# Kernel tuning notes

Measured on AMD Instinct MI355X. Metric: run time of the kernel, lower is better.

Reference implementation:

```python
import jax, jax.numpy as jnp
import numpy as np


def setup_inputs() -> dict:
    key = jax.random.key(0)
    k1, k2, k3 = jax.random.split(key, 3)
    B, Cin, Cout, K, H, W = 4, 64, 64, 3, 160, 160
    inputs = jax.random.normal(k1, (B, Cin, H, W), dtype=jnp.float32)
    # fractional dilation rates in [1, 3]
    rate_map = 1.0 + 2.0 * jax.random.uniform(k2, (B, 1, H, W), dtype=jnp.float32)
    # xavier-uniform-ish init
    limit = float(np.sqrt(6.0 / (Cin * K * K + Cout * K * K)))
    weight = jax.random.uniform(k3, (Cout, Cin, K, K), dtype=jnp.float32,
                                minval=-limit, maxval=limit)
    bias = jnp.zeros((Cout,), dtype=jnp.float32)
    return {"inputs": inputs, "weight": weight, "rate_map": rate_map,
            "bias": bias, "stride_h": 1, "stride_w": 1}


def _pdconv2d(inputs, weight, rate_map, bias, stride_h, stride_w):
    """Perspective (fractional, per-pixel) dilated conv with same padding.

    For each output pixel, the KxK taps are placed at center + offset*rate,
    where rate comes from rate_map and may be fractional -> bilinear sampling
    with zeros outside the image.
    """
    B, C, H, W = inputs.shape
    O, _, K, _ = weight.shape
    HO = (H + stride_h - 1) // stride_h
    WO = (W + stride_w - 1) // stride_w

    rate = rate_map[:, 0, ::stride_h, ::stride_w]  # [B,HO,WO]
    cy = (jnp.arange(HO) * stride_h).astype(jnp.float32)
    cx = (jnp.arange(WO) * stride_w).astype(jnp.float32)
    off = jnp.arange(K, dtype=jnp.float32) - (K - 1) / 2.0  # centered taps

    # sampling coords [B,HO,WO,K,K]
    sy = cy[None, :, None, None, None] + off[None, None, None, :, None] * rate[:, :, :, None, None]
    sx = cx[None, None, :, None, None] + off[None, None, None, None, :] * rate[:, :, :, None, None]
    sy = jnp.broadcast_to(sy, (B, HO, WO, K, K))
    sx = jnpp = jnp.broadcast_to(sx, (B, HO, WO, K, K))
    sx = jnp_p = sx  # no-op alias (keeps names clear)

    y0 = jnp.floor(sy)
    x0 = jnp.floor(sx)
    wy = sy - y0  # bilinear weights
    wx = sx - x0
    y0i = y0.astype(jnp.int32)
    x0i = x0.astype(jnp.int32)

    img = inputs.reshape(B, C, H * W)

    def gather(idx):  # idx [B,HO,WO,K,K] -> [B,C,HO,WO,K,K]
        return jax.vmap(lambda im, ix: jnp.take(im, ix, axis=-1))(img, idx)

    acc = jnp.zeros((B, C, HO, WO, K, K), dtype=inputs.dtype)
    corners = [(0, 0, (1 - wy) * (1 - wx)), (0, 1, (1 - wy) * wx),
               (1, 0, wy * (1 - wx)), (1, 1, wy * wx)]
    for dy, dx, cw in corners:
        yy = y0i + dy
        xx = x0i + dx
        valid = (yy >= 0) & (yy < H) & (xx >= 0) & (xx < W)
        idx = jnp.clip(yy, 0, H - 1) * W + jnp.clip(xx, 0, W - 1)
        w = (cw * valid.astype(inputs.dtype))[:, None]  # [B,1,HO,WO,K,K]
        acc = acc + gather(idx) * w

    # [B,C,HO,WO,K,K] x [O,C,K,K] -> [B,O,HO,WO]
    out = jnp.einsum('bchwkl,ockl->bohw', acc, weight)
    return out + bias[None, :, None, None]


def reference(inputs, weight, rate_map, bias, stride_h, stride_w):
    return _pdconv2d(inputs, weight, rate_map, bias, stride_h, stride_w)
```

## Files before the change

kernel.cpp:

```cpp
#include <hip/hip_runtime.h>
#include <hip/hip_bf16.h>

#define NB   4
#define CIN  64
#define COUT 64
#define HH   160
#define WW   160
#define HW   (HH * WW)

#define RT   8
#define CT   22
#define RS   72
#define RSB  (RS * 2)
#define HIN_SHORTS (RT * CT * RS)

typedef __attribute__((ext_vector_type(8))) short bf16x8;
typedef __attribute__((ext_vector_type(4))) float f32x4;
typedef __attribute__((ext_vector_type(2))) float f32x2;
typedef __attribute__((ext_vector_type(4))) unsigned int u32x4;

static __device__ __forceinline__ short f2bf(float v) {
    return __builtin_bit_cast(short, __float2bfloat16(v));
}

__global__ void wtf_kernel(const float* __restrict__ w, short* __restrict__ wtf) {
    int i = blockIdx.x * 256 + threadIdx.x;
    if (i < 36864) {
        const int j  = i & 7;
        const int l  = (i >> 3) & 63;
        const int mt = (i >> 9) & 3;
        const int ks = (i >> 11) & 1;
        const int t  = i >> 12;
        const int o  = 16 * mt + (l & 15);
        const int c  = 32 * ks + 8 * (l >> 4) + j;
        wtf[i] = f2bf(w[(o * CIN + c) * 9 + t]);
    }
}

static __device__ __forceinline__ void consume_tap(
    const u32x4 v00, const u32x4 v01, const u32x4 v10, const u32x4 v11,
    const float c00, const float c01, const float c10, const float c11,
    const bf16x8 wf0, const bf16x8 wf1, const bf16x8 wf2, const bf16x8 wf3,
    f32x4 acc[4])
{
    union { bf16x8 v; unsigned u[4]; } pf;
#pragma unroll
    for (int wd = 0; wd < 4; ++wd) {
        f32x2 s;
        {
            const unsigned u0 = v00[wd];
            const f32x2 xv = { __builtin_bit_cast(float, u0 << 16),
                               __builtin_bit_cast(float, u0 & 0xffff0000u) };
            s = c00 * xv;
        }
        {
            const unsigned u0 = v01[wd];
            const f32x2 xv = { __builtin_bit_cast(float, u0 << 16),
                               __builtin_bit_cast(float, u0 & 0xffff0000u) };
            s += c01 * xv;
        }
        {
            const unsigned u0 = v10[wd];
            const f32x2 xv = { __builtin_bit_cast(float, u0 << 16),
                               __builtin_bit_cast(float, u0 & 0xffff0000u) };
            s += c10 * xv;
        }
        {
            const unsigned u0 = v11[wd];
            const f32x2 xv = { __builtin_bit_cast(float, u0 << 16),
                               __builtin_bit_cast(float, u0 & 0xffff0000u) };
            s += c11 * xv;
        }
        unsigned r;
        asm("v_cvt_pk_bf16_f32 %0, %1, %2" : "=v"(r) : "v"(s.x), "v"(s.y));
        pf.u[wd] = r;
    }
    acc[0] = __builtin_amdgcn_mfma_f32_16x16x32_bf16(wf0, pf.v, acc[0], 0, 0, 0);
    acc[1] = __builtin_amdgcn_mfma_f32_16x16x32_bf16(wf1, pf.v, acc[1], 0, 0, 0);
    acc[2] = __builtin_amdgcn_mfma_f32_16x16x32_bf16(wf2, pf.v, acc[2], 0, 0, 0);
    acc[3] = __builtin_amdgcn_mfma_f32_16x16x32_bf16(wf3, pf.v, acc[3], 0, 0, 0);
}

__global__ __launch_bounds__(256, 4) void pdconv_tile_kernel(
    const float* __restrict__ in,
    const short* __restrict__ wtf,
    const float* __restrict__ rate_map,
    const float* __restrict__ bias,
    float* __restrict__ out)
{
    __shared__ short hin[HIN_SHORTS];
    __shared__ float red[2][64][17];

    const int tid  = threadIdx.x;
    const int wave = tid >> 6;
    const int lane = tid & 63;
    const int px   = lane & 15;
    const int g    = lane >> 4;
    const int r    = wave >> 1;
    const int th   = wave & 1;

    const int cpx = gridDim.x >> 3;
    const int bid = (blockIdx.x & 7) * cpx + (blockIdx.x >> 3);

    const int b   = bid / 800;
    const int rem = bid - b * 800;
    const int rr  = rem / 10;
    const int cc  = rem - rr * 10;
    const int oy  = 2 * rr - 3;
    const int ox  = 16 * cc - 3;

    if (tid < RT * CT) {
        const int ty = tid / CT;
        const int tx = tid - ty * CT;
        const int gy = min(max(oy + ty, 0), HH - 1);
        const int gx = min(max(ox + tx, 0), WW - 1);
        const float* src = in + (size_t)b * CIN * HW + gy * WW + gx;
        short* dst = hin + tid * RS;
#pragma unroll 16
        for (int c = 0; c < CIN; ++c)
            dst[c] = f2bf(src[(size_t)c * HW]);
    }

    const int row = 2 * rr + r;
    const int x   = 16 * cc + px;
    const float rate = rate_map[b * HW + row * WW + x];
    const float fy = (float)row, fx = (float)x;

    float wy0v[3], wy1v[3];  int ryb[3];
#pragma unroll
    for (int ky = 0; ky < 3; ++ky) {
        const float sy  = fy + (float)(ky - 1) * rate;
        const float y0f = floorf(sy);
        const float wy  = sy - y0f;
        const int   y0  = (int)y0f;
        const float vy0 = (y0 >= 0 && y0 < HH) ? 1.0f : 0.0f;
        const float vy1 = (y0 + 1 >= 0 && y0 + 1 < HH) ? 1.0f : 0.0f;
        wy0v[ky] = (1.0f - wy) * vy0;
        wy1v[ky] = wy * vy1;
        ryb[ky]  = (y0 - oy) * (CT * RSB);
    }
    float wx0v[3], wx1v[3];  int txb[3];
#pragma unroll
    for (int kx = 0; kx < 3; ++kx) {
        const float sx  = fx + (float)(kx - 1) * rate;
        const float x0f = floorf(sx);
        const float wx  = sx - x0f;
        const int   x0  = (int)x0f;
        const float vx0 = (x0 >= 0 && x0 < WW) ? 1.0f : 0.0f;
        const float vx1 = (x0 + 1 >= 0 && x0 + 1 < WW) ? 1.0f : 0.0f;
        wx0v[kx] = (1.0f - wx) * vx0;
        wx1v[kx] = wx * vx1;
        txb[kx]  = (x0 - ox) * RSB;
    }

    const int chan_off = 32 * th + 8 * g;

    const short* wtb = wtf + lane * 8;

    f32x4 acc[4];
#pragma unroll
    for (int mt = 0; mt < 4; ++mt) acc[mt] = (f32x4){0.f, 0.f, 0.f, 0.f};

    __syncthreads();

#define DO_TAP(T) do {                                                       \
    const int ky = (T) / 3, kx = (T) - 3 * ((T) / 3);         \
    const float c00 = wy0v[ky] * wx0v[kx];                                   \
    const float c01 = wy0v[ky] * wx1v[kx];                                   \
    const float c10 = wy1v[ky] * wx0v[kx];                                   \
    const float c11 = wy1v[ky] * wx1v[kx];                                   \
    const short* hk = (const short*)((const char*)hin + ryb[ky] + txb[kx])   \
                      + chan_off;                                            \
    const u32x4 v00 = *(const u32x4*)(hk);                                   \
    const u32x4 v01 = *(const u32x4*)(hk + RS);                              \
    const u32x4 v10 = *(const u32x4*)(hk + CT * RS);                         \
    const u32x4 v11 = *(const u32x4*)(hk + (CT + 1) * RS);                   \
    const short* wb = wtb + (size_t)(((T) * 2 + th) * 4) * 512;              \
    const bf16x8 wf0 = *(const bf16x8*)(wb);                                 \
    const bf16x8 wf1 = *(const bf16x8*)(wb + 512);                           \
    const bf16x8 wf2 = *(const bf16x8*)(wb + 1024);                          \
    const bf16x8 wf3 = *(const bf16x8*)(wb + 1536);                          \
    consume_tap(v00, v01, v10, v11, c00, c01, c10, c11,                      \
                wf0, wf1, wf2, wf3, acc);                                    \
} while (0)

    DO_TAP(0); DO_TAP(1); DO_TAP(2); DO_TAP(3); DO_TAP(4);
    DO_TAP(5); DO_TAP(6); DO_TAP(7); DO_TAP(8);
#undef DO_TAP

    if (th == 1) {
#pragma unroll
        for (int mt = 0; mt < 4; ++mt)
#pragma unroll
            for (int j = 0; j < 4; ++j)
                red[r][lane][4 * mt + j] = acc[mt][j];
    }
    __syncthreads();
    if (th == 0) {
        float* op = out + (size_t)b * COUT * HW + row * WW + 16 * cc + px;
#pragma unroll
        for (int mt = 0; mt < 4; ++mt) {
            const f32x4 bv = *(const f32x4*)(bias + 16 * mt + 4 * g);
#pragma unroll
            for (int j = 0; j < 4; ++j) {
                const int o = 16 * mt + 4 * g + j;
                op[(size_t)o * HW] = acc[mt][j] + red[r][lane][4 * mt + j]
                                   + bv[j];
            }
        }
    }
}

__global__ void wt2_kernel(const float* __restrict__ w, short* __restrict__ wt2) {
    int i = blockIdx.x * 256 + threadIdx.x;
    if (i < 9 * COUT * CIN) {
        int c = i & 63, o = (i >> 6) & 63, t = i >> 12;
        wt2[i] = f2bf(w[(o * CIN + c) * 9 + t]);
    }
}

__global__ __launch_bounds__(256) void pdconv_mfma_kernel(
    const float* __restrict__ in, const short* __restrict__ wt2,
    const float* __restrict__ rate_map, const float* __restrict__ bias,
    float* __restrict__ out)
{
    const int tid = threadIdx.x, wave = tid >> 6, lane = tid & 63;
    const int px = lane & 15, g = lane >> 4;
    const int cpx = gridDim.x >> 3;
    const int bid = (blockIdx.x & 7) * cpx + (blockIdx.x >> 3);
    const int base = bid * 64 + wave * 16;
    const int b = base / HW, pix0 = base - b * HW;
    const int y = pix0 / WW, x0 = pix0 - y * WW, x = x0 + px;
    const float rate = rate_map[base + px];
    const float fy = (float)y, fx = (float)x;
    f32x4 acc[4];
#pragma unroll
    for (int mt = 0; mt < 4; ++mt) acc[mt] = (f32x4){0.f, 0.f, 0.f, 0.f};
    const float* img  = in + (size_t)b * CIN * HW;
    const float* imgg = img + (size_t)g * 8 * HW;
#pragma unroll 1
    for (int t = 0; t < 9; ++t) {
        const int ky = t / 3, kx = t - 3 * ky;
        const float sy = fy + (float)(ky - 1) * rate;
        const float sx = fx + (float)(kx - 1) * rate;
        const float y0f = floorf(sy), x0f = floorf(sx);
        const float wy = sy - y0f, wx = sx - x0f;
        const int y0 = (int)y0f, x0i = (int)x0f, y1 = y0 + 1, x1 = x0i + 1;
        const float omwy = 1.0f - wy, omwx = 1.0f - wx;
        const float vy0 = (y0 >= 0 && y0 < HH) ? 1.0f : 0.0f;
        const float vy1 = (y1 >= 0 && y1 < HH) ? 1.0f : 0.0f;
        const float vx0 = (x0i >= 0 && x0i < WW) ? 1.0f : 0.0f;
        const float vx1 = (x1 >= 0 && x1 < WW) ? 1.0f : 0.0f;
        const float c00 = omwy * omwx * vy0 * vx0, c01 = omwy * wx * vy0 * vx1;
        const float c10 = wy * omwx * vy1 * vx0,  c11 = wy * wx * vy1 * vx1;
        const int cy0 = min(max(y0, 0), HH - 1), cy1 = min(max(y1, 0), HH - 1);
        const int cx0 = min(max(x0i, 0), WW - 1), cx1 = min(max(x1, 0), WW - 1);
        const int i00 = cy0 * WW + cx0, i01 = cy0 * WW + cx1;
        const int i10 = cy1 * WW + cx0, i11 = cy1 * WW + cx1;
#pragma unroll
        for (int ks = 0; ks < 2; ++ks) {
            bf16x8 wf[4];
#pragma unroll
            for (int mt = 0; mt < 4; ++mt)
                wf[mt] = *(const bf16x8*)(wt2 +
                          ((t * COUT + 16 * mt + px) * CIN + 32 * ks + 8 * g));
            float a[8];
#pragma unroll
            for (int j = 0; j < 8; ++j) {
                const float* ch = imgg + (size_t)(32 * ks + j) * HW;
                a[j] = c00 * ch[i00] + c01 * ch[i01] + c10 * ch[i10] + c11 * ch[i11];
            }
            union { bf16x8 v; short s[8]; } pf;
#pragma unroll
            for (int j = 0; j < 8; ++j) pf.s[j] = f2bf(a[j]);
#pragma unroll
            for (int mt = 0; mt < 4; ++mt)
                acc[mt] = __builtin_amdgcn_mfma_f32_16x16x32_bf16(
                              wf[mt], pf.v, acc[mt], 0, 0, 0);
        }
    }
    float* op = out + (size_t)b * COUT * HW + pix0 + px;
#pragma unroll
    for (int mt = 0; mt < 4; ++mt)
#pragma unroll
        for (int r = 0; r < 4; ++r) {
            const int o = 16 * mt + 4 * g + r;
            op[(size_t)o * HW] = acc[mt][r] + bias[o];
        }
}

extern "C" void kernel_launch(void* const* d_in, const int* in_sizes, int n_in,
                              void* d_out, int out_size, void* d_ws, size_t ws_size,
                              hipStream_t stream) {
    (void)in_sizes; (void)n_in; (void)out_size;
    const float* in   = (const float*)d_in[0];
    const float* w    = (const float*)d_in[1];
    const float* rm   = (const float*)d_in[2];
    const float* bias = (const float*)d_in[3];
    float* out = (float*)d_out;

    const size_t WTF_BYTES = 36864 * sizeof(short);

    if (ws_size >= WTF_BYTES) {
        short* wtf = (short*)d_ws;
        hipLaunchKernelGGL(wtf_kernel, dim3(144), dim3(256), 0, stream, w, wtf);
        const int nblocks = NB * 80 * 10;
        hipLaunchKernelGGL(pdconv_tile_kernel, dim3(nblocks), dim3(256), 0,
                           stream, in, wtf, rm, bias, out);
    } else {
        short* wt2 = (short*)d_ws;
        hipLaunchKernelGGL(wt2_kernel, dim3(144), dim3(256), 0, stream, w, wt2);
        hipLaunchKernelGGL(pdconv_mfma_kernel, dim3((NB * HW) / 64), dim3(256),
                           0, stream, in, wt2, rm, bias, out);
    }
}
```

Measured before the change: 43.42 us.

## Double tile width per block to reuse staged halo and weight fragments

Each block now computes a 2x32 output tile instead of 2x16, staging a wider 8x38 bf16 halo in shared memory. Each tap's weight fragments are loaded once and applied to two 16-pixel sub-tiles, which halves weight reloads and cuts the halo overhead per output pixel. The staging loop also packs channel pairs with v_cvt_pk_bf16_f32 and writes 16-byte vectors to shared memory instead of single shorts. In exchange, the block count halves and register use and LDS per block rise (launch bounds lowered to 2 waves/SIMD), which reduces occupancy and latency hiding.

```diff
diff --git a/kernel.cpp b/kernel.cpp
--- a/kernel.cpp
+++ b/kernel.cpp
@@ -9,7 +9,7 @@
 #define HW   (HH * WW)
 
 #define RT   8
-#define CT   22
+#define CT   38
 #define RS   72
 #define RSB  (RS * 2)
 #define HIN_SHORTS (RT * CT * RS)
@@ -81,7 +81,7 @@
     acc[3] = __builtin_amdgcn_mfma_f32_16x16x32_bf16(wf3, pf.v, acc[3], 0, 0, 0);
 }
 
-__global__ __launch_bounds__(256, 4) void pdconv_tile_kernel(
+__global__ __launch_bounds__(256, 2) void pdconv_pair_kernel(
     const float* __restrict__ in,
     const short* __restrict__ wtf,
     const float* __restrict__ rate_map,
@@ -89,7 +89,7 @@
     float* __restrict__ out)
 {
     __shared__ short hin[HIN_SHORTS];
-    __shared__ float red[2][64][17];
+    __shared__ float red[2][2][64][17];
 
     const int tid  = threadIdx.x;
     const int wave = tid >> 6;
@@ -102,86 +102,126 @@
     const int cpx = gridDim.x >> 3;
     const int bid = (blockIdx.x & 7) * cpx + (blockIdx.x >> 3);
 
-    const int b   = bid / 800;
-    const int rem = bid - b * 800;
-    const int rr  = rem / 10;
-    const int cc  = rem - rr * 10;
+    const int b   = bid / 400;
+    const int rem = bid - b * 400;
+    const int rr  = rem / 5;
+    const int cc  = rem - rr * 5;
     const int oy  = 2 * rr - 3;
-    const int ox  = 16 * cc - 3;
-
-    if (tid < RT * CT) {
-        const int ty = tid / CT;
-        const int tx = tid - ty * CT;
-        const int gy = min(max(oy + ty, 0), HH - 1);
-        const int gx = min(max(ox + tx, 0), WW - 1);
-        const float* src = in + (size_t)b * CIN * HW + gy * WW + gx;
-        short* dst = hin + tid * RS;
-#pragma unroll 16
-        for (int c = 0; c < CIN; ++c)
-            dst[c] = f2bf(src[(size_t)c * HW]);
-    }
-
-    const int row = 2 * rr + r;
-    const int x   = 16 * cc + px;
-    const float rate = rate_map[b * HW + row * WW + x];
-    const float fy = (float)row, fx = (float)x;
-
-    float wy0v[3], wy1v[3];  int ryb[3];
-#pragma unroll
-    for (int ky = 0; ky < 3; ++ky) {
-        const float sy  = fy + (float)(ky - 1) * rate;
-        const float y0f = floorf(sy);
-        const float wy  = sy - y0f;
-        const int   y0  = (int)y0f;
-        const float vy0 = (y0 >= 0 && y0 < HH) ? 1.0f : 0.0f;
-        const float vy1 = (y0 + 1 >= 0 && y0 + 1 < HH) ? 1.0f : 0.0f;
-        wy0v[ky] = (1.0f - wy) * vy0;
-        wy1v[ky] = wy * vy1;
-        ryb[ky]  = (y0 - oy) * (CT * RSB);
-    }
-    float wx0v[3], wx1v[3];  int txb[3];
-#pragma unroll
-    for (int kx = 0; kx < 3; ++kx) {
-        const float sx  = fx + (float)(kx - 1) * rate;
-        const float x0f = floorf(sx);
-        const float wx  = sx - x0f;
-        const int   x0  = (int)x0f;
-        const float vx0 = (x0 >= 0 && x0 < WW) ? 1.0f : 0.0f;
-        const float vx1 = (x0 + 1 >= 0 && x0 + 1 < WW) ? 1.0f : 0.0f;
-        wx0v[kx] = (1.0f - wx) * vx0;
-        wx1v[kx] = wx * vx1;
-        txb[kx]  = (x0 - ox) * RSB;
+    const int ox  = 32 * cc - 3;
+
+    const float* ibase = in + (size_t)b * CIN * HW;
+#pragma unroll
+    for (int it = 0; it < 2; ++it) {
+        const int rec = it * 256 + tid;
+        if (rec < RT * CT) {
+            const int ty = rec / CT;
+            const int tx = rec - ty * CT;
+            const int gy = min(max(oy + ty, 0), HH - 1);
+            const int gx = min(max(ox + tx, 0), WW - 1);
+            const float* src = ibase + gy * WW + gx;
+            short* dst = hin + rec * RS;
+#pragma unroll
+            for (int co = 0; co < 8; ++co) {
+                union { u32x4 v; unsigned u[4]; } pk;
+#pragma unroll
+                for (int q = 0; q < 4; ++q) {
+                    const float lo = src[(size_t)(co * 8 + 2 * q)     * HW];
+                    const float hi = src[(size_t)(co * 8 + 2 * q + 1) * HW];
+                    unsigned pr;
+                    asm("v_cvt_pk_bf16_f32 %0, %1, %2"
+                        : "=v"(pr) : "v"(lo), "v"(hi));
+                    pk.u[q] = pr;
+                }
+                *(u32x4*)(dst + co * 8) = pk.v;
+            }
+        }
+    }
+
+    const int row  = 2 * rr + r;
+    const int col0 = 32 * cc;
+    const float rate0 = rate_map[b * HW + row * WW + col0 + px];
+    const float rate1 = rate_map[b * HW + row * WW + col0 + 16 + px];
+    const float fy  = (float)row;
+    const float fx0 = (float)(col0 + px);
+    const float fx1 = (float)(col0 + 16 + px);
+
+    float wy0v[2][3], wy1v[2][3], wx0v[2][3], wx1v[2][3];
+    int   ryb[2][3], txb[2][3];
+#pragma unroll
+    for (int s = 0; s < 2; ++s) {
+        const float rate = s ? rate1 : rate0;
+        const float fx   = s ? fx1   : fx0;
+#pragma unroll
+        for (int k = 0; k < 3; ++k) {
+            const float sy  = fy + (float)(k - 1) * rate;
+            const float y0f = floorf(sy);
+            const float wy  = sy - y0f;
+            const int   y0  = (int)y0f;
+            const float vy0 = (y0 >= 0 && y0 < HH) ? 1.0f : 0.0f;
+            const float vy1 = (y0 + 1 >= 0 && y0 + 1 < HH) ? 1.0f : 0.0f;
+            wy0v[s][k] = (1.0f - wy) * vy0;
+            wy1v[s][k] = wy * vy1;
+            ryb[s][k]  = (y0 - oy) * (CT * RSB);
+
+            const float sx  = fx + (float)(k - 1) * rate;
+            const float x0f = floorf(sx);
+            const float wx  = sx - x0f;
+            const int   x0  = (int)x0f;
+            const float vx0 = (x0 >= 0 && x0 < WW) ? 1.0f : 0.0f;
+            const float vx1 = (x0 + 1 >= 0 && x0 + 1 < WW) ? 1.0f : 0.0f;
+            wx0v[s][k] = (1.0f - wx) * vx0;
+            wx1v[s][k] = wx * vx1;
+            txb[s][k]  = (x0 - ox) * RSB;
+        }
     }
 
     const int chan_off = 32 * th + 8 * g;
-
     const short* wtb = wtf + lane * 8;
 
-    f32x4 acc[4];
-#pragma unroll
-    for (int mt = 0; mt < 4; ++mt) acc[mt] = (f32x4){0.f, 0.f, 0.f, 0.f};
+    f32x4 acc0[4], acc1[4];
+#pragma unroll
+    for (int mt = 0; mt < 4; ++mt) {
+        acc0[mt] = (f32x4){0.f, 0.f, 0.f, 0.f};
+        acc1[mt] = (f32x4){0.f, 0.f, 0.f, 0.f};
+    }
 
     __syncthreads();
 
 #define DO_TAP(T) do {                                                       \
     const int ky = (T) / 3, kx = (T) - 3 * ((T) / 3);         \
-    const float c00 = wy0v[ky] * wx0v[kx];                                   \
-    const float c01 = wy0v[ky] * wx1v[kx];                                   \
-    const float c10 = wy1v[ky] * wx0v[kx];                                   \
-    const float c11 = wy1v[ky] * wx1v[kx];                                   \
-    const short* hk = (const short*)((const char*)hin + ryb[ky] + txb[kx])   \
-                      + chan_off;                                            \
-    const u32x4 v00 = *(const u32x4*)(hk);                                   \
-    const u32x4 v01 = *(const u32x4*)(hk + RS);                              \
-    const u32x4 v10 = *(const u32x4*)(hk + CT * RS);                         \
-    const u32x4 v11 = *(const u32x4*)(hk + (CT + 1) * RS);                   \
     const short* wb = wtb + (size_t)(((T) * 2 + th) * 4) * 512;              \
     const bf16x8 wf0 = *(const bf16x8*)(wb);                                 \
     const bf16x8 wf1 = *(const bf16x8*)(wb + 512);                           \
     const bf16x8 wf2 = *(const bf16x8*)(wb + 1024);                          \
     const bf16x8 wf3 = *(const bf16x8*)(wb + 1536);                          \
-    consume_tap(v00, v01, v10, v11, c00, c01, c10, c11,                      \
-                wf0, wf1, wf2, wf3, acc);                                    \
+    {                                                           \
+        const float c00 = wy0v[0][ky] * wx0v[0][kx];                         \
+        const float c01 = wy0v[0][ky] * wx1v[0][kx];                         \
+        const float c10 = wy1v[0][ky] * wx0v[0][kx];                         \
+        const float c11 = wy1v[0][ky] * wx1v[0][kx];                         \
+        const short* hk = (const short*)((const char*)hin                    \
+                          + ryb[0][ky] + txb[0][kx]) + chan_off;             \
+        const u32x4 v00 = *(const u32x4*)(hk);                               \
+        const u32x4 v01 = *(const u32x4*)(hk + RS);                          \
+        const u32x4 v10 = *(const u32x4*)(hk + CT * RS);                     \
+        const u32x4 v11 = *(const u32x4*)(hk + (CT + 1) * RS);               \
+        consume_tap(v00, v01, v10, v11, c00, c01, c10, c11,                  \
+                    wf0, wf1, wf2, wf3, acc0);                               \
+    }                                                                        \
+    {                                            \
+        const float c00 = wy0v[1][ky] * wx0v[1][kx];                         \
+        const float c01 = wy0v[1][ky] * wx1v[1][kx];                         \
+        const float c10 = wy1v[1][ky] * wx0v[1][kx];                         \
+        const float c11 = wy1v[1][ky] * wx1v[1][kx];                         \
+        const short* hk = (const short*)((const char*)hin                    \
+                          + ryb[1][ky] + txb[1][kx]) + chan_off;             \
+        const u32x4 v00 = *(const u32x4*)(hk);                               \
+        const u32x4 v01 = *(const u32x4*)(hk + RS);                          \
+        const u32x4 v10 = *(const u32x4*)(hk + CT * RS);                     \
+        const u32x4 v11 = *(const u32x4*)(hk + (CT + 1) * RS);               \
+        consume_tap(v00, v01, v10, v11, c00, c01, c10, c11,                  \
+                    wf0, wf1, wf2, wf3, acc1);                               \
+    }                                                                        \
 } while (0)
 
     DO_TAP(0); DO_TAP(1); DO_TAP(2); DO_TAP(3); DO_TAP(4);
@@ -192,20 +232,23 @@
 #pragma unroll
         for (int mt = 0; mt < 4; ++mt)
 #pragma unroll
-            for (int j = 0; j < 4; ++j)
-                red[r][lane][4 * mt + j] = acc[mt][j];
+            for (int j = 0; j < 4; ++j) {
+                red[0][r][lane][4 * mt + j] = acc0[mt][j];
+                red[1][r][lane][4 * mt + j] = acc1[mt][j];
+            }
     }
     __syncthreads();
     if (th == 0) {
-        float* op = out + (size_t)b * COUT * HW + row * WW + 16 * cc + px;
+        float* op0 = out + (size_t)b * COUT * HW + row * WW + col0 + px;
+        float* op1 = op0 + 16;
 #pragma unroll
         for (int mt = 0; mt < 4; ++mt) {
             const f32x4 bv = *(const f32x4*)(bias + 16 * mt + 4 * g);
 #pragma unroll
             for (int j = 0; j < 4; ++j) {
                 const int o = 16 * mt + 4 * g + j;
-                op[(size_t)o * HW] = acc[mt][j] + red[r][lane][4 * mt + j]
-                                   + bv[j];
+                op0[(size_t)o * HW] = acc0[mt][j] + red[0][r][lane][4 * mt + j] + bv[j];
+                op1[(size_t)o * HW] = acc1[mt][j] + red[1][r][lane][4 * mt + j] + bv[j];
             }
         }
     }
@@ -304,8 +347,8 @@
     if (ws_size >= WTF_BYTES) {
         short* wtf = (short*)d_ws;
         hipLaunchKernelGGL(wtf_kernel, dim3(144), dim3(256), 0, stream, w, wtf);
-        const int nblocks = NB * 80 * 10;
-        hipLaunchKernelGGL(pdconv_tile_kernel, dim3(nblocks), dim3(256), 0,
+        const int nblocks = NB * 80 * 5;
+        hipLaunchKernelGGL(pdconv_pair_kernel, dim3(nblocks), dim3(256), 0,
                            stream, in, wtf, rm, bias, out);
     } else {
         short* wt2 = (short*)d_ws;
```

After: 46.76 us. 1.08x slower.

## Give each wave a full output row and drop split-K LDS reduction

Applied to the files above, without the earlier changes.

Each block now covers four output rows of 16 pixels instead of two, so the shared halo tile grows from 8 to 10 rows and the grid is halved. Each wave handles all 64 input channels for its own row, looping over two channel halves per tap, instead of two waves splitting the channels. This removes the shared-memory partial-sum reduction and the second barrier, and cuts redundant halo loads per output. In exchange each wave does twice the serial MFMA and bilinear work, and fewer blocks may lower parallelism and latency hiding.

```diff
diff --git a/kernel.cpp b/kernel.cpp
--- a/kernel.cpp
+++ b/kernel.cpp
@@ -8,7 +8,7 @@
 #define WW   160
 #define HW   (HH * WW)
 
-#define RT   8
+#define RT   10
 #define CT   22
 #define RS   72
 #define RSB  (RS * 2)
@@ -81,7 +81,7 @@
     acc[3] = __builtin_amdgcn_mfma_f32_16x16x32_bf16(wf3, pf.v, acc[3], 0, 0, 0);
 }
 
-__global__ __launch_bounds__(256, 4) void pdconv_tile_kernel(
+__global__ __launch_bounds__(256, 4) void pdconv_quad_kernel(
     const float* __restrict__ in,
     const short* __restrict__ wtf,
     const float* __restrict__ rate_map,
@@ -89,24 +89,21 @@
     float* __restrict__ out)
 {
     __shared__ short hin[HIN_SHORTS];
-    __shared__ float red[2][64][17];
 
     const int tid  = threadIdx.x;
     const int wave = tid >> 6;
     const int lane = tid & 63;
     const int px   = lane & 15;
     const int g    = lane >> 4;
-    const int r    = wave >> 1;
-    const int th   = wave & 1;
 
     const int cpx = gridDim.x >> 3;
     const int bid = (blockIdx.x & 7) * cpx + (blockIdx.x >> 3);
 
-    const int b   = bid / 800;
-    const int rem = bid - b * 800;
+    const int b   = bid / 400;
+    const int rem = bid - b * 400;
     const int rr  = rem / 10;
     const int cc  = rem - rr * 10;
-    const int oy  = 2 * rr - 3;
+    const int oy  = 4 * rr - 3;
     const int ox  = 16 * cc - 3;
 
     if (tid < RT * CT) {
@@ -121,7 +118,7 @@
             dst[c] = f2bf(src[(size_t)c * HW]);
     }
 
-    const int row = 2 * rr + r;
+    const int row = 4 * rr + wave;
     const int x   = 16 * cc + px;
     const float rate = rate_map[b * HW + row * WW + x];
     const float fy = (float)row, fx = (float)x;
@@ -153,8 +150,7 @@
         txb[kx]  = (x0 - ox) * RSB;
     }
 
-    const int chan_off = 32 * th + 8 * g;
-
+    const int chan_off = 8 * g;
     const short* wtb = wtf + lane * 8;
 
     f32x4 acc[4];
@@ -169,44 +165,37 @@
     const float c01 = wy0v[ky] * wx1v[kx];                                   \
     const float c10 = wy1v[ky] * wx0v[kx];                                   \
     const float c11 = wy1v[ky] * wx1v[kx];                                   \
-    const short* hk = (const short*)((const char*)hin + ryb[ky] + txb[kx])   \
+    const short* hb = (const short*)((const char*)hin + ryb[ky] + txb[kx])   \
                       + chan_off;                                            \
-    const u32x4 v00 = *(const u32x4*)(hk);                                   \
-    const u32x4 v01 = *(const u32x4*)(hk + RS);                              \
-    const u32x4 v10 = *(const u32x4*)(hk + CT * RS);                         \
-    const u32x4 v11 = *(const u32x4*)(hk + (CT + 1) * RS);                   \
-    const short* wb = wtb + (size_t)(((T) * 2 + th) * 4) * 512;              \
-    const bf16x8 wf0 = *(const bf16x8*)(wb);                                 \
-    const bf16x8 wf1 = *(const bf16x8*)(wb + 512);                           \
-    const bf16x8 wf2 = *(const bf16x8*)(wb + 1024);                          \
-    const bf16x8 wf3 = *(const bf16x8*)(wb + 1536);                          \
-    consume_tap(v00, v01, v10, v11, c00, c01, c10, c11,                      \
-                wf0, wf1, wf2, wf3, acc);                                    \
+    _Pragma("unroll")                                                        \
+    for (int ks = 0; ks < 2; ++ks) {                                         \
+        const short* hk = hb + 32 * ks;                                      \
+        const u32x4 v00 = *(const u32x4*)(hk);                               \
+        const u32x4 v01 = *(const u32x4*)(hk + RS);                          \
+        const u32x4 v10 = *(const u32x4*)(hk + CT * RS);                     \
+        const u32x4 v11 = *(const u32x4*)(hk + (CT + 1) * RS);               \
+        const short* wb = wtb + (size_t)(((T) * 2 + ks) * 4) * 512;          \
+        const bf16x8 wf0 = *(const bf16x8*)(wb);                             \
+        const bf16x8 wf1 = *(const bf16x8*)(wb + 512);                       \
+        const bf16x8 wf2 = *(const bf16x8*)(wb + 1024);                      \
+        const bf16x8 wf3 = *(const bf16x8*)(wb + 1536);                      \
+        consume_tap(v00, v01, v10, v11, c00, c01, c10, c11,                  \
+                    wf0, wf1, wf2, wf3, acc);                                \
+    }                                                                        \
 } while (0)
 
     DO_TAP(0); DO_TAP(1); DO_TAP(2); DO_TAP(3); DO_TAP(4);
     DO_TAP(5); DO_TAP(6); DO_TAP(7); DO_TAP(8);
 #undef DO_TAP
 
-    if (th == 1) {
-#pragma unroll
-        for (int mt = 0; mt < 4; ++mt)
-#pragma unroll
-            for (int j = 0; j < 4; ++j)
-                red[r][lane][4 * mt + j] = acc[mt][j];
-    }
-    __syncthreads();
-    if (th == 0) {
-        float* op = out + (size_t)b * COUT * HW + row * WW + 16 * cc + px;
-#pragma unroll
-        for (int mt = 0; mt < 4; ++mt) {
-            const f32x4 bv = *(const f32x4*)(bias + 16 * mt + 4 * g);
-#pragma unroll
-            for (int j = 0; j < 4; ++j) {
-                const int o = 16 * mt + 4 * g + j;
-                op[(size_t)o * HW] = acc[mt][j] + red[r][lane][4 * mt + j]
-                                   + bv[j];
-            }
+    float* op = out + (size_t)b * COUT * HW + row * WW + 16 * cc + px;
+#pragma unroll
+    for (int mt = 0; mt < 4; ++mt) {
+        const f32x4 bv = *(const f32x4*)(bias + 16 * mt + 4 * g);
+#pragma unroll
+        for (int j = 0; j < 4; ++j) {
+            const int o = 16 * mt + 4 * g + j;
+            op[(size_t)o * HW] = acc[mt][j] + bv[j];
         }
     }
 }
@@ -304,8 +293,8 @@
     if (ws_size >= WTF_BYTES) {
         short* wtf = (short*)d_ws;
         hipLaunchKernelGGL(wtf_kernel, dim3(144), dim3(256), 0, stream, w, wtf);
-        const int nblocks = NB * 80 * 10;
-        hipLaunchKernelGGL(pdconv_tile_kernel, dim3(nblocks), dim3(256), 0,
+        const int nblocks = NB * 40 * 10;
+        hipLaunchKernelGGL(pdconv_quad_kernel, dim3(nblocks), dim3(256), 0,
                            stream, in, wtf, rm, bias, out);
     } else {
         short* wt2 = (short*)d_ws;
```

After: 41.66 us (median of 3 runs). 1.04x faster.
